# Optimization experiments

Hardware: AMD Instinct MI355X
Metric: run time of the kernel (lower is better)

The kernel has to match this reference:

```python
import jax, jax.numpy as jnp
import numpy as np

NUM_HEADS = 12

def setup_inputs() -> dict:
    key = jax.random.key(0)
    k1, k2, k3, k4 = jax.random.split(key, 4)
    B, N, C = 8, 1024, 768
    x = jax.random.normal(k1, (B, N, C), dtype=jnp.float32)
    # torch nn.Linear weights are [out_features, in_features]
    qkv_w = jax.random.normal(k2, (3 * C, C), dtype=jnp.float32) * (1.0 / np.sqrt(C))
    proj_w = jax.random.normal(k3, (C, C), dtype=jnp.float32) * (1.0 / np.sqrt(C))
    proj_b = jax.random.normal(k4, (C,), dtype=jnp.float32) * 0.02
    return {"x": x, "qkv_w": qkv_w, "proj_w": proj_w, "proj_b": proj_b}

def reference(x, qkv_w, proj_w, proj_b):
    B, N, C = x.shape
    H = NUM_HEADS
    D = C // H
    scale = D ** -0.5
    # qkv: [B, N, 3C] -> [3, B, H, N, D]
    qkv = jnp.einsum('bnc,oc->bno', x, qkv_w)
    qkv = qkv.reshape(B, N, 3, H, D).transpose(2, 0, 3, 1, 4)
    q, k, v = qkv[0], qkv[1], qkv[2]
    attn = jnp.einsum('bhnd,bhmd->bhnm', q, k) * scale  # [B,H,N,N]
    attn = jax.nn.softmax(attn, axis=-1)
    # attn_drop is identity at eval (p=0.0)
    out = jnp.einsum('bhnm,bhmd->bhnd', attn, v)  # [B,H,N,D]
    out = out.transpose(0, 2, 1, 3).reshape(B, N, C)
    out = jnp.einsum('bnc,oc->bno', out, proj_w) + proj_b
    # proj_drop is identity at eval (p=0.0)
    return (out, attn)
```

## Files before the change

### kernel.cpp

```cpp
#include <hip/hip_runtime.h>

typedef unsigned short u16;
typedef u16 us8 __attribute__((ext_vector_type(8)));
typedef u16 us4 __attribute__((ext_vector_type(4)));
typedef __bf16 bf16x8 __attribute__((ext_vector_type(8)));
typedef __bf16 bf16x4 __attribute__((ext_vector_type(4)));
typedef float f32x4 __attribute__((ext_vector_type(4)));

static __device__ __forceinline__ u16 f2bf(float f) {
  unsigned int u = __builtin_bit_cast(unsigned int, f);
  u += 0x7fffu + ((u >> 16) & 1u);
  return (u16)(u >> 16);
}

static __device__ __forceinline__ void gload16(const void* g, void* l) {
  __builtin_amdgcn_global_load_lds((const __attribute__((address_space(1))) void*)g,
                                   (__attribute__((address_space(3))) void*)l,
                                   16, 0, 0);
}

static __device__ __forceinline__ bf16x8 ldfrag_g(const u16* p) {
  return __builtin_bit_cast(bf16x8, *(const us8*)p);
}

template <int N> static __device__ __forceinline__ void vmwait() {
  asm volatile("s_waitcnt vmcnt(%0)" :: "n"(N) : "memory");
}

__global__ void cvt_all(const float* __restrict__ x, const float* __restrict__ wq,
                        const float* __restrict__ wp, u16* __restrict__ xb,
                        u16* __restrict__ wqb, u16* __restrict__ wpb) {
  int i = blockIdx.x * blockDim.x + threadIdx.x;
  const float* s; u16* d; int off;
  if (i < 786432)       { s = x;  d = xb;  off = i; }
  else if (i < 1007616) { s = wq; d = wqb; off = i - 786432; }
  else                  { s = wp; d = wpb; off = i - 1007616; }
  const float4* sp = (const float4*)s + (size_t)off * 2;
  float4 a = sp[0], b = sp[1];
  us8 o;
  o[0] = f2bf(a.x); o[1] = f2bf(a.y); o[2] = f2bf(a.z); o[3] = f2bf(a.w);
  o[4] = f2bf(b.x); o[5] = f2bf(b.y); o[6] = f2bf(b.z); o[7] = f2bf(b.w);
  *((us8*)d + off) = o;
}

template <bool STORE_BF16, bool ADD_BIAS>
__global__ __launch_bounds__(256, 2) void gemm_bt(
    const u16* __restrict__ A, const u16* __restrict__ Bt,
    void* __restrict__ Cout, const float* __restrict__ bias, int Ncols) {
  __shared__ __align__(16) u16 As[128 * 64];
  __shared__ __align__(16) u16 Bs[128 * 64];
  const int tid = threadIdx.x;
  const int w = tid >> 6, l = tid & 63;
  const int fr = l & 15, fq = l >> 4;
  const int row0 = blockIdx.x * 128;
  const int col0 = blockIdx.y * 128;
  const int wr = (w >> 1) * 64, wc = (w & 1) * 64;
  const int lrow = l >> 3;
  const int lcol = (l & 7) * 8;

  f32x4 acc[4][4];
#pragma unroll
  for (int m = 0; m < 4; ++m)
#pragma unroll
    for (int n = 0; n < 4; ++n) acc[m][n] = f32x4{0.f, 0.f, 0.f, 0.f};

  for (int kt = 0; kt < 12; ++kt) {
    const int k0 = kt * 64;
    __syncthreads();
#pragma unroll
    for (int i = 0; i < 4; ++i) {
      int c = w * 4 + i;
      gload16(A  + (size_t)(row0 + c * 8 + lrow) * 768 + k0 + lcol, &As[c * 512]);
      gload16(Bt + (size_t)(col0 + c * 8 + lrow) * 768 + k0 + lcol, &Bs[c * 512]);
    }
    __syncthreads();
#pragma unroll
    for (int kk = 0; kk < 2; ++kk) {
      bf16x8 a[4], b[4];
#pragma unroll
      for (int m = 0; m < 4; ++m)
        a[m] = __builtin_bit_cast(bf16x8, *(const us8*)&As[(wr + m * 16 + fr) * 64 + kk * 32 + fq * 8]);
#pragma unroll
      for (int n = 0; n < 4; ++n)
        b[n] = __builtin_bit_cast(bf16x8, *(const us8*)&Bs[(wc + n * 16 + fr) * 64 + kk * 32 + fq * 8]);
#pragma unroll
      for (int m = 0; m < 4; ++m)
#pragma unroll
        for (int n = 0; n < 4; ++n)
          acc[m][n] = __builtin_amdgcn_mfma_f32_16x16x32_bf16(a[m], b[n], acc[m][n], 0, 0, 0);
    }
  }

#pragma unroll
  for (int m = 0; m < 4; ++m) {
    int r = row0 + wr + m * 16 + fq * 4;
#pragma unroll
    for (int n = 0; n < 4; ++n) {
      int c = col0 + wc + n * 16 + fr;
#pragma unroll
      for (int j = 0; j < 4; ++j) {
        float v = acc[m][n][j];
        if (STORE_BF16) {
          ((u16*)Cout)[(size_t)(r + j) * Ncols + c] = f2bf(v);
        } else {
          float o = ADD_BIAS ? v + bias[c] : v;
          ((float*)Cout)[(size_t)(r + j) * Ncols + c] = o;
        }
      }
    }
  }
}

__global__ void transpose_v(const u16* __restrict__ qkv, u16* __restrict__ vt) {
  __shared__ __align__(16) u16 s[64][72];
  const int bh = blockIdx.x >> 4;
  const int nt = blockIdx.x & 15;
  const int b = bh / 12, h = bh - b * 12;
  const int n0 = nt * 64;
  const int tid = threadIdx.x;
#pragma unroll
  for (int it = 0; it < 2; ++it) {
    int idx = tid + it * 256;
    int r = idx >> 3, c8 = (idx & 7) * 8;
    us8 v = *(const us8*)&qkv[(size_t)(b * 1024 + n0 + r) * 2304 + 1536 + h * 64 + c8];
    *(us8*)&s[r][c8] = v;
  }
  __syncthreads();
#pragma unroll
  for (int it = 0; it < 2; ++it) {
    int idx = tid + it * 256;
    int d = idx >> 3, n8 = (idx & 7) * 8;
    us8 o;
#pragma unroll
    for (int i = 0; i < 8; ++i) o[i] = s[n8 + i][d];
    *(us8*)&vt[(size_t)(bh * 64 + d) * 1024 + n0 + n8] = o;
  }
}

__global__ __launch_bounds__(256, 2) void attn_fused(
    const u16* __restrict__ qkv, const u16* __restrict__ vt,
    float* __restrict__ attn_out, u16* __restrict__ ctx) {
  __shared__ __align__(16) u16 P[32 * 1024];
  __shared__ float red[2][4][32];
  const int tid = threadIdx.x;
  const int w = tid >> 6, l = tid & 63;
  const int fr = l & 15, fq = l >> 4;
  const int bh = blockIdx.x >> 5;
  const int qt = blockIdx.x & 31;
  const int b = bh / 12, h = bh - b * 12;
  const int q0 = qt * 32;

  bf16x8 aq[2][2];
#pragma unroll
  for (int m = 0; m < 2; ++m)
#pragma unroll
    for (int kk = 0; kk < 2; ++kk)
      aq[m][kk] = ldfrag_g(&qkv[(size_t)(b * 1024 + q0 + m * 16 + fr) * 2304 + h * 64 + kk * 32 + fq * 8]);
  vmwait<0>();
  __builtin_amdgcn_sched_barrier(0);

  char* kbase = (char*)P + w * 16384;
  const int kl = l >> 3;
  const int csrc = ((l & 7) ^ (kl & 7)) * 8;
  const u16* kb = &qkv[(size_t)b * 1024 * 2304 + 768 + h * 64];
  const u16* ksrc = kb + (size_t)(w * 256 + kl) * 2304 + csrc;

  f32x4 acc[16][2];
#pragma unroll
  for (int n = 0; n < 16; ++n)
#pragma unroll
    for (int m = 0; m < 2; ++m) acc[n][m] = f32x4{0.f, 0.f, 0.f, 0.f};

#pragma unroll
  for (int i = 0; i < 8; ++i)
    gload16(ksrc + (size_t)(i * 8) * 2304, kbase + i * 1024);

#pragma unroll
  for (int g = 0; g < 4; ++g) {
    if (g < 3) {
#pragma unroll
      for (int i = 0; i < 8; ++i)
        gload16(ksrc + (size_t)((g + 1) * 64 + i * 8) * 2304,
                kbase + ((g + 1) & 1) * 8192 + i * 1024);
      vmwait<8>();
    } else {
      vmwait<0>();
    }
    __builtin_amdgcn_sched_barrier(0);
    char* buf = kbase + (g & 1) * 8192;
    __builtin_amdgcn_s_setprio(1);
#pragma unroll
    for (int n2 = 0; n2 < 4; ++n2) {
      int rowb = (n2 * 16 + fr) * 128;
#pragma unroll
      for (int kk = 0; kk < 2; ++kk) {
        int cidx = (kk * 4 + fq) ^ (fr & 7);
        bf16x8 bk = __builtin_bit_cast(bf16x8, *(const us8*)(buf + rowb + cidx * 16));
        int n = g * 4 + n2;
        acc[n][0] = __builtin_amdgcn_mfma_f32_16x16x32_bf16(bk, aq[0][kk], acc[n][0], 0, 0, 0);
        acc[n][1] = __builtin_amdgcn_mfma_f32_16x16x32_bf16(bk, aq[1][kk], acc[n][1], 0, 0, 0);
      }
    }
    __builtin_amdgcn_s_setprio(0);
  }

  float mx[2];
#pragma unroll
  for (int m = 0; m < 2; ++m) mx[m] = -3.4e38f;
#pragma unroll
  for (int n = 0; n < 16; ++n)
#pragma unroll
    for (int m = 0; m < 2; ++m) {
      f32x4 v = acc[n][m];
      mx[m] = fmaxf(mx[m], fmaxf(fmaxf(v[0], v[1]), fmaxf(v[2], v[3])));
    }
#pragma unroll
  for (int m = 0; m < 2; ++m) {
    float v = mx[m];
    v = fmaxf(v, __shfl_xor(v, 16));
    v = fmaxf(v, __shfl_xor(v, 32));
    mx[m] = v;
  }
  if (fq == 0) {
#pragma unroll
    for (int m = 0; m < 2; ++m) red[0][w][m * 16 + fr] = mx[m];
  }
  __syncthreads();
  const float C = 0.125f * 1.44269504f;
  float nrm[2];
#pragma unroll
  for (int m = 0; m < 2; ++m) {
    int r = m * 16 + fr;
    float rm = fmaxf(fmaxf(red[0][0][r], red[0][1][r]), fmaxf(red[0][2][r], red[0][3][r]));
    nrm[m] = -rm * C;
  }

  float sum[2] = {0.f, 0.f};
#pragma unroll
  for (int n = 0; n < 16; ++n)
#pragma unroll
    for (int m = 0; m < 2; ++m) {
#pragma unroll
      for (int j = 0; j < 4; ++j) {
        float p = exp2f(fmaf(acc[n][m][j], C, nrm[m]));
        acc[n][m][j] = p;
        sum[m] += p;
      }
    }
#pragma unroll
  for (int m = 0; m < 2; ++m) {
    float v = sum[m];
    v += __shfl_xor(v, 16);
    v += __shfl_xor(v, 32);
    sum[m] = v;
  }
  if (fq == 0) {
#pragma unroll
    for (int m = 0; m < 2; ++m) red[1][w][m * 16 + fr] = sum[m];
  }
  __syncthreads();
  float rinv[2];
#pragma unroll
  for (int m = 0; m < 2; ++m) {
    int r = m * 16 + fr;
    rinv[m] = 1.0f / (red[1][0][r] + red[1][1][r] + red[1][2][r] + red[1][3][r]);
  }

  float* aout = attn_out + (size_t)bh * (1024 * 1024) + (size_t)q0 * 1024 + w * 256;
#pragma unroll
  for (int n = 0; n < 16; ++n)
#pragma unroll
    for (int m = 0; m < 2; ++m) {
      int row = m * 16 + fr;
      int key = n * 16 + fq * 4;
      f32x4 v = acc[n][m];
      f32x4 pv;
      pv[0] = v[0] * rinv[m]; pv[1] = v[1] * rinv[m];
      pv[2] = v[2] * rinv[m]; pv[3] = v[3] * rinv[m];
      __builtin_nontemporal_store(pv, (f32x4*)(aout + (size_t)row * 1024 + key));
      bf16x4 pk;
      pk[0] = (__bf16)pv[0]; pk[1] = (__bf16)pv[1];
      pk[2] = (__bf16)pv[2]; pk[3] = (__bf16)pv[3];
      int byte = (row * 2048 + (w * 256 + key) * 2) ^ ((row & 7) << 4);
      *(us4*)((char*)P + byte) = __builtin_bit_cast(us4, pk);
    }
  __syncthreads();

  f32x4 o2[2];
  o2[0] = f32x4{0.f, 0.f, 0.f, 0.f};
  o2[1] = f32x4{0.f, 0.f, 0.f, 0.f};
  const u16* vb = &vt[(size_t)bh * 64 * 1024 + (size_t)(w * 16 + fr) * 1024];
#pragma unroll 8
  for (int ks = 0; ks < 32; ++ks) {
    bf16x8 bv = ldfrag_g(&vb[ks * 32 + fq * 8]);
#pragma unroll
    for (int m = 0; m < 2; ++m) {
      int row = m * 16 + fr;
      int byte = (row * 2048 + (ks * 32 + fq * 8) * 2) ^ ((row & 7) << 4);
      bf16x8 ap = __builtin_bit_cast(bf16x8, *(const us8*)((const char*)P + byte));
      o2[m] = __builtin_amdgcn_mfma_f32_16x16x32_bf16(ap, bv, o2[m], 0, 0, 0);
    }
  }
#pragma unroll
  for (int m = 0; m < 2; ++m)
#pragma unroll
    for (int j = 0; j < 4; ++j) {
      int row = q0 + m * 16 + fq * 4 + j;
      int col = h * 64 + w * 16 + fr;
      ctx[(size_t)(b * 1024 + row) * 768 + col] = f2bf(o2[m][j]);
    }
}

extern "C" void kernel_launch(void* const* d_in, const int* in_sizes, int n_in,
                              void* d_out, int out_size, void* d_ws, size_t ws_size,
                              hipStream_t stream) {
  const float* x      = (const float*)d_in[0];
  const float* qkv_w  = (const float*)d_in[1];
  const float* proj_w = (const float*)d_in[2];
  const float* proj_b = (const float*)d_in[3];
  float* out = (float*)d_out;
  float* attn_out = out + 6291456;

  char* ws = (char*)d_ws;
  u16* qkv_bf = (u16*)(ws);
  u16* x_bf   = (u16*)(ws + 37748736);
  u16* wq_bf  = (u16*)(ws + 50331648);
  u16* wp_bf  = (u16*)(ws + 53870592);
  u16* vt_bf  = (u16*)(ws + 55050240);
  u16* ctx_bf = (u16*)(ws + 67633152);

  cvt_all<<<4224, 256, 0, stream>>>(x, qkv_w, proj_w, x_bf, wq_bf, wp_bf);

  gemm_bt<true, false><<<dim3(64, 18), 256, 0, stream>>>(x_bf, wq_bf, qkv_bf, nullptr, 2304);
  transpose_v<<<1536, 256, 0, stream>>>(qkv_bf, vt_bf);
  attn_fused<<<3072, 256, 0, stream>>>(qkv_bf, vt_bf, attn_out, ctx_bf);
  gemm_bt<false, true><<<dim3(64, 6), 256, 0, stream>>>(ctx_bf, wp_bf, out, proj_b, 768);
}
```

Baseline: 223.6 us.

## Double-buffer GEMM LDS tiles and vectorize epilogue stores via swapped MFMA operands

The GEMM kernel now keeps two LDS buffers per operand and issues the global-to-LDS loads for the next K tile before computing on the current one, with one barrier per iteration instead of two. This is meant to overlap memory latency with MFMA work. The MFMA operands are swapped so each lane holds four consecutive columns, which lets the epilogue write 4-wide vector stores and load the bias as a vector. It also raises MFMA issue priority with setprio. LDS use doubles to 64KB per block, which may limit occupancy to fewer blocks per CU.

```diff
diff --git a/kernel.cpp b/kernel.cpp
--- a/kernel.cpp
+++ b/kernel.cpp
@@ -47,8 +47,8 @@
 __global__ __launch_bounds__(256, 2) void gemm_bt(
     const u16* __restrict__ A, const u16* __restrict__ Bt,
     void* __restrict__ Cout, const float* __restrict__ bias, int Ncols) {
-  __shared__ __align__(16) u16 As[128 * 64];
-  __shared__ __align__(16) u16 Bs[128 * 64];
+  __shared__ __align__(16) u16 As[2][128 * 64];
+  __shared__ __align__(16) u16 Bs[2][128 * 64];
   const int tid = threadIdx.x;
   const int w = tid >> 6, l = tid & 63;
   const int fr = l & 15, fq = l >> 4;
@@ -58,54 +58,70 @@
   const int lrow = l >> 3;
   const int lcol = (l & 7) * 8;
 
+  const u16* Ab = A  + (size_t)(row0 + w * 32 + lrow) * 768 + lcol;
+  const u16* Bb = Bt + (size_t)(col0 + w * 32 + lrow) * 768 + lcol;
+
   f32x4 acc[4][4];
 #pragma unroll
   for (int m = 0; m < 4; ++m)
 #pragma unroll
     for (int n = 0; n < 4; ++n) acc[m][n] = f32x4{0.f, 0.f, 0.f, 0.f};
 
+#pragma unroll
+  for (int i = 0; i < 4; ++i) {
+    gload16(Ab + (size_t)(i * 8) * 768, &As[0][(w * 4 + i) * 512]);
+    gload16(Bb + (size_t)(i * 8) * 768, &Bs[0][(w * 4 + i) * 512]);
+  }
+  __syncthreads();
+
   for (int kt = 0; kt < 12; ++kt) {
-    const int k0 = kt * 64;
-    __syncthreads();
-#pragma unroll
-    for (int i = 0; i < 4; ++i) {
-      int c = w * 4 + i;
-      gload16(A  + (size_t)(row0 + c * 8 + lrow) * 768 + k0 + lcol, &As[c * 512]);
-      gload16(Bt + (size_t)(col0 + c * 8 + lrow) * 768 + k0 + lcol, &Bs[c * 512]);
-    }
-    __syncthreads();
+    const int cur = kt & 1;
+    if (kt < 11) {
+      const int k1 = (kt + 1) * 64;
+#pragma unroll
+      for (int i = 0; i < 4; ++i) {
+        gload16(Ab + (size_t)(i * 8) * 768 + k1, &As[cur ^ 1][(w * 4 + i) * 512]);
+        gload16(Bb + (size_t)(i * 8) * 768 + k1, &Bs[cur ^ 1][(w * 4 + i) * 512]);
+      }
+    }
 #pragma unroll
     for (int kk = 0; kk < 2; ++kk) {
       bf16x8 a[4], b[4];
 #pragma unroll
       for (int m = 0; m < 4; ++m)
-        a[m] = __builtin_bit_cast(bf16x8, *(const us8*)&As[(wr + m * 16 + fr) * 64 + kk * 32 + fq * 8]);
+        a[m] = __builtin_bit_cast(bf16x8, *(const us8*)&As[cur][(wr + m * 16 + fr) * 64 + kk * 32 + fq * 8]);
 #pragma unroll
       for (int n = 0; n < 4; ++n)
-        b[n] = __builtin_bit_cast(bf16x8, *(const us8*)&Bs[(wc + n * 16 + fr) * 64 + kk * 32 + fq * 8]);
+        b[n] = __builtin_bit_cast(bf16x8, *(const us8*)&Bs[cur][(wc + n * 16 + fr) * 64 + kk * 32 + fq * 8]);
+      __builtin_amdgcn_s_setprio(1);
 #pragma unroll
       for (int m = 0; m < 4; ++m)
 #pragma unroll
         for (int n = 0; n < 4; ++n)
-          acc[m][n] = __builtin_amdgcn_mfma_f32_16x16x32_bf16(a[m], b[n], acc[m][n], 0, 0, 0);
-    }
+          acc[m][n] = __builtin_amdgcn_mfma_f32_16x16x32_bf16(b[n], a[m], acc[m][n], 0, 0, 0);
+      __builtin_amdgcn_s_setprio(0);
+    }
+    __syncthreads();
   }
 
 #pragma unroll
   for (int m = 0; m < 4; ++m) {
-    int r = row0 + wr + m * 16 + fq * 4;
+    const int r = row0 + wr + m * 16 + fr;
 #pragma unroll
     for (int n = 0; n < 4; ++n) {
-      int c = col0 + wc + n * 16 + fr;
-#pragma unroll
-      for (int j = 0; j < 4; ++j) {
-        float v = acc[m][n][j];
-        if (STORE_BF16) {
-          ((u16*)Cout)[(size_t)(r + j) * Ncols + c] = f2bf(v);
-        } else {
-          float o = ADD_BIAS ? v + bias[c] : v;
-          ((float*)Cout)[(size_t)(r + j) * Ncols + c] = o;
+      const int cc = col0 + wc + n * 16 + fq * 4;
+      f32x4 v = acc[m][n];
+      if (STORE_BF16) {
+        us4 o;
+        o[0] = f2bf(v[0]); o[1] = f2bf(v[1]); o[2] = f2bf(v[2]); o[3] = f2bf(v[3]);
+        *(us4*)((u16*)Cout + (size_t)r * Ncols + cc) = o;
+      } else {
+        f32x4 o = v;
+        if (ADD_BIAS) {
+          f32x4 bb = *(const f32x4*)&bias[cc];
+          o[0] += bb[0]; o[1] += bb[1]; o[2] += bb[2]; o[3] += bb[3];
         }
+        *(f32x4*)((float*)Cout + (size_t)r * Ncols + cc) = o;
       }
     }
   }
```

Result: slower. 238.3 us (+6.6%).
